# Optimization experiments

Hardware: AMD Instinct MI355X
Metric: run time of the kernel (lower is better)

The kernel has to match this reference:

```python
import jax, jax.numpy as jnp
import numpy as np

EPS = 1e-12  # torch F.normalize default eps


def conv1x1(x, w, b):
    # x: [N,C,H,W], w: [K,C], b: [K]
    return jnp.einsum('nchw,kc->nkhw', x, w) + b[None, :, None, None]


def forward_sa(f1, f2, cw1, cb1, cw2, cb2):
    n, _, h, w = f1.shape
    c1 = conv1x1(f1, cw1, cb1)  # [N,1,H,W]
    c2 = conv1x1(f2, cw2, cb2)
    c1 = jax.nn.softmax(c1.reshape(n, h * w), axis=1).reshape(n, 1, h, w)
    c2 = jax.nn.softmax(c2.reshape(n, h * w), axis=1).reshape(n, 1, h, w)
    return c1 * f1, c2 * f2


def l2norm_ch(x):
    # torch F.normalize(x) -> p=2 over dim=1 with eps clamp
    n = jnp.sqrt(jnp.sum(x * x, axis=1, keepdims=True))
    return x / jnp.maximum(n, EPS)


def forward_ca(f1, f2, pw1, pb1, pw2, pb2):
    N, C, H, W = f1.shape
    f1_cl = conv1x1(f1, pw1, pb1).reshape(N, -1, H * W)  # [N,Cl,HW]
    f2_cl = conv1x1(f2, pw2, pb2).reshape(N, -1, H * W)
    # A[n,p,q] = sum_c f2_cl[n,c,p] * f1_cl[n,c,q]  -> [N,HW,HW]
    A_c = jnp.tanh(jnp.einsum('ncp,ncq->npq', f2_cl, f1_cl))
    f1_v = f1.reshape(N, C, H * W)
    f2_v = f2.reshape(N, C, H * W)
    # f1_hat = f1_v @ A_c^T ; f2_hat = f2_v @ A_c
    f1_hat = jnp.einsum('ncp,nqp->ncq', f1_v, A_c).reshape(N, C, H, W)
    f2_hat = jnp.einsum('ncp,npq->ncq', f2_v, A_c).reshape(N, C, H, W)
    return l2norm_ch(f1_hat), l2norm_ch(f2_hat)


def setup_inputs() -> dict:
    key = jax.random.key(0)
    ks = jax.random.split(key, 10)
    N, C, H, W = 2, 256, 64, 64
    Cl = C // 16
    sc = 1.0 / np.sqrt(C)
    return {
        'f1': jax.random.normal(ks[0], (N, C, H, W), jnp.float32),
        'f2': jax.random.normal(ks[1], (N, C, H, W), jnp.float32),
        'pw1': jax.random.normal(ks[2], (Cl, C), jnp.float32) * sc,
        'pb1': jax.random.normal(ks[3], (Cl,), jnp.float32) * sc,
        'pw2': jax.random.normal(ks[4], (Cl, C), jnp.float32) * sc,
        'pb2': jax.random.normal(ks[5], (Cl,), jnp.float32) * sc,
        'cw1': jax.random.normal(ks[6], (1, C), jnp.float32) * sc,
        'cb1': jax.random.normal(ks[7], (1,), jnp.float32) * sc,
        'cw2': jax.random.normal(ks[8], (1, C), jnp.float32) * sc,
        'cb2': jax.random.normal(ks[9], (1,), jnp.float32) * sc,
    }


def reference(f1, f2, pw1, pb1, pw2, pb2, cw1, cb1, cw2, cb2):
    f1_1, f2_1 = forward_sa(f1, f2, cw1, cb1, cw2, cb2)
    f1_hat, f2_hat = forward_ca(f1_1, f2_1, pw1, pb1, pw2, pb2)
    fp1_hat = jax.nn.relu(f1_hat + f1)
    fp2_hat = jax.nn.relu(f2_hat + f2)
    f1_2, f2_2 = forward_sa(fp1_hat, fp2_hat, cw1, cb1, cw2, cb2)
    # Original calls forward_ca(f1_2, f2_2) again but discards the result
    # and returns (f1_2, f2_2); the dead call is omitted (identical output).
    return (f1_2, f2_2)
```

## Files before the change

kernel.cpp:

```cpp
#include <hip/hip_runtime.h>
#include <hip/hip_bf16.h>
#include <math.h>

#define N_B 2
#define C_CH 256
#define HW_SZ 4096
#define CL_CH 16

typedef __bf16 bf16x8 __attribute__((ext_vector_type(8)));
typedef float f32x4 __attribute__((ext_vector_type(4)));
typedef float f32x16 __attribute__((ext_vector_type(16)));

__device__ __forceinline__ unsigned short f2bf(float x){
  __hip_bfloat16 b = __float2bfloat16(x);
  return *reinterpret_cast<unsigned short*>(&b);
}
__device__ __forceinline__ unsigned int cvtpk(float a, float b){
  unsigned int r;
  asm("v_cvt_pk_bf16_f32 %0, %1, %2" : "=v"(r) : "v"(a), "v"(b));
  return r;
}
__device__ __forceinline__ float tanh_fast(float x){
  float e = __expf(2.0f * x);
  return fmaf(-2.0f, __builtin_amdgcn_rcpf(1.0f + e), 1.0f);
}
__device__ __forceinline__ void gload16(const void* gsrc, void* lds_dst){
  __builtin_amdgcn_global_load_lds(
      (const __attribute__((address_space(1))) unsigned int*)gsrc,
      (__attribute__((address_space(3))) unsigned int*)lds_dst, 16, 0, 0);
}

__global__ void k_conv1(const float* __restrict__ f1, const float* __restrict__ f2,
                        const float* __restrict__ w1, const float* __restrict__ w2,
                        const float* __restrict__ b1, const float* __restrict__ b2,
                        float* __restrict__ cv){
  const int i = blockIdx.z, n = blockIdx.y, t = threadIdx.x;
  const int ql = t & 63, cg = t >> 6;
  const int q = blockIdx.x * 64 + ql;
  const float* f = (i ? f2 : f1) + n * C_CH * HW_SZ;
  const float* w = i ? w2 : w1;
  __shared__ float ws[C_CH];
  __shared__ float red[4][72];
  ws[t] = w[t];
  __syncthreads();
  float acc = 0.f;
  #pragma unroll 8
  for (int c = cg * 64; c < cg * 64 + 64; ++c)
    acc += f[c * HW_SZ + q] * ws[c];
  red[cg][ql] = acc;
  __syncthreads();
  if (t < 64){
    float s = red[0][t] + red[1][t] + red[2][t] + red[3][t] + (i ? b2[0] : b1[0]);
    cv[(i * 2 + n) * HW_SZ + blockIdx.x * 64 + t] = s;
  }
}

__global__ void k_softmax(const float* __restrict__ cv, float* __restrict__ pr){
  const int r = blockIdx.x, t = threadIdx.x;
  const float* x = cv + r * HW_SZ;
  float* y = pr + r * HW_SZ;
  __shared__ float red[256];
  float v[16];
  float m = -1e30f;
  #pragma unroll
  for (int j = 0; j < 16; j++){ v[j] = x[j * 256 + t]; m = fmaxf(m, v[j]); }
  red[t] = m; __syncthreads();
  for (int s = 128; s > 0; s >>= 1){ if (t < s) red[t] = fmaxf(red[t], red[t + s]); __syncthreads(); }
  m = red[0]; __syncthreads();
  float sum = 0.f;
  #pragma unroll
  for (int j = 0; j < 16; j++){ v[j] = __expf(v[j] - m); sum += v[j]; }
  red[t] = sum; __syncthreads();
  for (int s = 128; s > 0; s >>= 1){ if (t < s) red[t] += red[t + s]; __syncthreads(); }
  const float inv = 1.0f / red[0];
  #pragma unroll
  for (int j = 0; j < 16; j++) y[j * 256 + t] = v[j] * inv;
}

__global__ void k_scale_cl(const float* __restrict__ f1, const float* __restrict__ f2,
                           const float* __restrict__ pr,
                           const float* __restrict__ pw1, const float* __restrict__ pw2,
                           const float* __restrict__ pb1, const float* __restrict__ pb2,
                           unsigned short* __restrict__ fs1, unsigned short* __restrict__ fs2,
                           unsigned short* __restrict__ clT1, unsigned short* __restrict__ clT2){
  const int i = blockIdx.z, n = blockIdx.y, t = threadIdx.x;
  const int ql = t & 63, cg = t >> 6;
  const int q = blockIdx.x * 64 + ql;
  const float* f = (i ? f2 : f1) + n * C_CH * HW_SZ;
  unsigned short* fs = (i ? fs2 : fs1) + n * C_CH * HW_SZ;
  unsigned short* clT = (i ? clT2 : clT1) + n * 32 * HW_SZ;
  const float* pw = i ? pw2 : pw1;
  const float* pb = i ? pb2 : pb1;
  __shared__ float wls[CL_CH * C_CH];
  __shared__ float red[4][CL_CH][66];
  #pragma unroll
  for (int j = 0; j < 16; j++) wls[j * 256 + t] = pw[j * 256 + t];
  __syncthreads();
  const float p = pr[(i * 2 + n) * HW_SZ + q];
  float acc[16];
  #pragma unroll
  for (int k = 0; k < 16; k++) acc[k] = 0.f;
  for (int c = cg * 64; c < cg * 64 + 64; ++c){
    float vv = f[c * HW_SZ + q] * p;
    fs[c * HW_SZ + q] = f2bf(vv);
    #pragma unroll
    for (int k = 0; k < 16; k++) acc[k] += wls[k * 256 + c] * vv;
  }
  #pragma unroll
  for (int k = 0; k < 16; k++) red[cg][k][ql] = acc[k];
  __syncthreads();
  #pragma unroll
  for (int j = 0; j < 4; j++){
    int e = j * 256 + t; int k = e >> 6, qq = e & 63;
    float s = red[0][k][qq] + red[1][k][qq] + red[2][k][qq] + red[3][k][qq] + pb[k];
    clT[(blockIdx.x * 64 + qq) * 32 + k] = f2bf(s);
  }
  if (t < 128){
    uint4 zv = {0u, 0u, 0u, 0u};
    int qq = t >> 1, half = t & 1;
    *reinterpret_cast<uint4*>(&clT[(blockIdx.x * 64 + qq) * 32 + 16 + half * 8]) = zv;
  }
}

__global__ __launch_bounds__(512, 4) void k_hat(
    const unsigned short* __restrict__ fs1, const unsigned short* __restrict__ fs2,
    const unsigned short* __restrict__ clT1, const unsigned short* __restrict__ clT2,
    float* __restrict__ hat1, float* __restrict__ hat2,
    float* __restrict__ pt1, float* __restrict__ pt2){
  const int t = threadIdx.x;
  const int bid = blockIdx.x;
  const int xcd = bid & 7, slot = bid >> 3;
  const int z = xcd >> 1;
  const int n = z & 1, i = z >> 1;
  const int x = slot * 2 + (xcd & 1);
  const int qt = x >> 1, ph = x & 1;
  const int q0 = qt * 64;
  const int pbase = ph * 2048;

  const unsigned short* fs = (i ? fs2 : fs1) + n * C_CH * HW_SZ;
  const unsigned short* uT = (i ? clT1 : clT2) + n * 32 * HW_SZ;
  const unsigned short* vT = (i ? clT2 : clT1) + n * 32 * HW_SZ;
  float* out = (ph ? (i ? pt2 : pt1) : (i ? hat2 : hat1)) + n * C_CH * HW_SZ;

  __shared__ __align__(16) unsigned short fsA[2][C_CH * 64];
  __shared__ __align__(16) unsigned short vB[2][64 * 32];
  __shared__ __align__(16) unsigned short aT[64 * 64];

  const int wv = t >> 6, l = t & 63;
  const int g4 = l >> 4, lr16 = l & 15;
  const int g2 = l >> 5, lr32 = l & 31;

  const int pfw = wv & 3;
  const int qf0 = (wv >> 2) * 2;
  const int cblk = wv & 3, qblk = wv >> 2;

  const bf16x8 ub0 = *reinterpret_cast<const bf16x8*>(&uT[(q0 + qf0 * 16 + lr16) * 32 + g4 * 8]);
  const bf16x8 ub1 = *reinterpret_cast<const bf16x8*>(&uT[(q0 + qf0 * 16 + 16 + lr16) * 32 + g4 * 8]);

  f32x16 acc0, acc1;
  #pragma unroll
  for (int r = 0; r < 16; ++r){ acc0[r] = 0.f; acc1[r] = 0.f; }
  const f32x4 zz = {0.f, 0.f, 0.f, 0.f};

  int fs_src[4];
  #pragma unroll
  for (int it = 0; it < 4; ++it){
    int d = it * 512 + t; int c = d >> 3, s = d & 7;
    int u = s ^ (c & 7) ^ (((c >> 3) & 1) << 2);
    fs_src[it] = c * (HW_SZ * 2) + u * 16;
  }
  int vt_src;
  {
    int j = t & 255; int p = j >> 2, s = j & 3;
    int u = s ^ (p & 3) ^ ((p >> 2) & 3);
    vt_src = p * 64 + u * 16;
  }
  int vbr;
  {
    int p = pfw * 16 + lr16;
    vbr = p * 64 + ((g4 ^ (p & 3) ^ ((p >> 2) & 3)) << 4);
  }
  unsigned atw0;
  {
    int qd = qf0 * 16 + lr16;
    int sw = (pfw * 2 + (g4 >> 1)) ^ (qd & 7) ^ (((qd >> 3) & 1) << 2);
    atw0 = qd * 128 + sw * 16 + (g4 & 1) * 8;
  }
  unsigned afo[2], bqo;
  #pragma unroll
  for (int cfi = 0; cfi < 2; ++cfi){
    int crow = cblk * 64 + cfi * 32 + lr32;
    afo[cfi] = crow * 128 + ((g2 ^ (crow & 7) ^ (((crow >> 3) & 1) << 2)) << 4);
  }
  {
    int qrow = qblk * 32 + lr32;
    bqo = qrow * 128 + ((g2 ^ (qrow & 7) ^ (((qrow >> 3) & 1) << 2)) << 4);
  }

  const char* fsb[2] = {(const char*)&fsA[0][0], (const char*)&fsA[1][0]};
  const char* vbb[2] = {(const char*)&vB[0][0], (const char*)&vB[1][0]};
  char* atb = (char*)&aT[0];

  auto stage_fs = [&](unsigned short* dstbase, int p0){
    const char* src = (const char*)fs + p0 * 2;
    #pragma unroll
    for (int it = 0; it < 4; ++it)
      gload16(src + fs_src[it], dstbase + (it * 512 + wv * 64) * 8);
  };
  auto stage_v = [&](unsigned short* dstbase, int p0){
    if (wv < 4)
      gload16((const char*)vT + p0 * 64 + vt_src, dstbase + wv * 512);
  };
  auto dgen = [&](const char* vbB){
    bf16x8 av = *reinterpret_cast<const bf16x8*>(vbB + vbr);
    f32x4 d0 = __builtin_amdgcn_mfma_f32_16x16x32_bf16(av, ub0, zz, 0, 0, 0);
    f32x4 d1 = __builtin_amdgcn_mfma_f32_16x16x32_bf16(av, ub1, zz, 0, 0, 0);
    uint2 pk;
    pk.x = cvtpk(tanh_fast(d0[0]), tanh_fast(d0[1]));
    pk.y = cvtpk(tanh_fast(d0[2]), tanh_fast(d0[3]));
    *reinterpret_cast<uint2*>(atb + atw0) = pk;
    pk.x = cvtpk(tanh_fast(d1[0]), tanh_fast(d1[1]));
    pk.y = cvtpk(tanh_fast(d1[2]), tanh_fast(d1[3]));
    *reinterpret_cast<uint2*>(atb + atw0 + 2048) = pk;
  };
  auto mmain = [&](const char* faB){
    #pragma unroll
    for (int ks = 0; ks < 4; ++ks){
      unsigned kx = (unsigned)(ks << 5);
      bf16x8 b0 = *reinterpret_cast<const bf16x8*>(atb + (bqo ^ kx));
      bf16x8 a0 = *reinterpret_cast<const bf16x8*>(faB + (afo[0] ^ kx));
      bf16x8 a1 = *reinterpret_cast<const bf16x8*>(faB + (afo[1] ^ kx));
      acc0 = __builtin_amdgcn_mfma_f32_32x32x16_bf16(a0, b0, acc0, 0, 0, 0);
      acc1 = __builtin_amdgcn_mfma_f32_32x32x16_bf16(a1, b0, acc1, 0, 0, 0);
    }
  };

  stage_fs(fsA[0], pbase);
  stage_v(vB[0], pbase);
  __syncthreads();

  #pragma unroll 1
  for (int k2 = 0; k2 < 16; ++k2){
    {
      const int p0n = pbase + (2 * k2 + 1) * 64;
      stage_fs(fsA[1], p0n);
      stage_v(vB[1], p0n);
      dgen(vbb[0]);
      asm volatile("s_waitcnt lgkmcnt(0)" ::: "memory");
      __builtin_amdgcn_sched_barrier(0);
      __builtin_amdgcn_s_barrier();
      mmain(fsb[0]);
      __syncthreads();
    }
    {
      const int p0n = pbase + (2 * k2 + 2) * 64;
      stage_fs(fsA[0], p0n);
      stage_v(vB[0], p0n);
      dgen(vbb[1]);
      asm volatile("s_waitcnt lgkmcnt(0)" ::: "memory");
      __builtin_amdgcn_sched_barrier(0);
      __builtin_amdgcn_s_barrier();
      mmain(fsb[1]);
      __syncthreads();
    }
  }

  const int qcol = q0 + qblk * 32 + lr32;
  #pragma unroll
  for (int r = 0; r < 16; ++r){
    int cr = (r & 3) + 8 * (r >> 2) + 4 * g2;
    out[(cblk * 64 + cr) * HW_SZ + qcol] = acc0[r];
    out[(cblk * 64 + 32 + cr) * HW_SZ + qcol] = acc1[r];
  }
}

__global__ void k_norm(float* __restrict__ hat1, float* __restrict__ hat2,
                       const float* __restrict__ pt1, const float* __restrict__ pt2,
                       const float* __restrict__ f1, const float* __restrict__ f2,
                       const float* __restrict__ cw1, const float* __restrict__ cw2,
                       const float* __restrict__ cb1, const float* __restrict__ cb2,
                       float* __restrict__ cv2){
  const int i = blockIdx.z, n = blockIdx.y, t = threadIdx.x;
  const int ql = t & 63, cg = t >> 6;
  const int q = blockIdx.x * 64 + ql;
  float* hat = (i ? hat2 : hat1) + n * C_CH * HW_SZ;
  const float* pt = (i ? pt2 : pt1) + n * C_CH * HW_SZ;
  const float* f = (i ? f2 : f1) + n * C_CH * HW_SZ;
  __shared__ float ws[C_CH];
  __shared__ float red[4][72];
  __shared__ float invs[64];
  ws[t] = (i ? cw2 : cw1)[t];
  __syncthreads();
  float s = 0.f;
  #pragma unroll 8
  for (int c = cg * 64; c < cg * 64 + 64; ++c){
    float h = hat[c * HW_SZ + q] + pt[c * HW_SZ + q];
    s += h * h;
  }
  red[cg][ql] = s; __syncthreads();
  if (t < 64){
    float ss = red[0][t] + red[1][t] + red[2][t] + red[3][t];
    invs[t] = 1.0f / fmaxf(sqrtf(ss), 1e-12f);
  }
  __syncthreads();
  const float inv = invs[ql];
  float ca = 0.f;
  #pragma unroll 8
  for (int c = cg * 64; c < cg * 64 + 64; ++c){
    float h = hat[c * HW_SZ + q] + pt[c * HW_SZ + q];
    float vv = fmaxf(h * inv + f[c * HW_SZ + q], 0.0f);
    hat[c * HW_SZ + q] = vv;
    ca += ws[c] * vv;
  }
  red[cg][ql] = ca; __syncthreads();
  if (t < 64){
    float ss = red[0][t] + red[1][t] + red[2][t] + red[3][t] + (i ? cb2[0] : cb1[0]);
    cv2[(i * 2 + n) * HW_SZ + blockIdx.x * 64 + t] = ss;
  }
}

__global__ void k_final(const float* __restrict__ fp1, const float* __restrict__ fp2,
                        const float* __restrict__ pr2, float* __restrict__ outp){
  const int i = blockIdx.z;
  const int idx4 = (blockIdx.x * 256 + threadIdx.x) * 4;
  const int n = idx4 >> 20;
  const int q = idx4 & (HW_SZ - 1);
  const float* fp = i ? fp2 : fp1;
  float4 vv = *reinterpret_cast<const float4*>(&fp[idx4]);
  float4 pp = *reinterpret_cast<const float4*>(&pr2[(i * 2 + n) * HW_SZ + q]);
  float4 o; o.x = vv.x * pp.x; o.y = vv.y * pp.y; o.z = vv.z * pp.z; o.w = vv.w * pp.w;
  *reinterpret_cast<float4*>(&outp[i * (C_CH * HW_SZ * N_B) + idx4]) = o;
}

extern "C" void kernel_launch(void* const* d_in, const int* in_sizes, int n_in,
                              void* d_out, int out_size, void* d_ws, size_t ws_size,
                              hipStream_t stream){
  const float* f1  = (const float*)d_in[0];
  const float* f2  = (const float*)d_in[1];
  const float* pw1 = (const float*)d_in[2];
  const float* pb1 = (const float*)d_in[3];
  const float* pw2 = (const float*)d_in[4];
  const float* pb2 = (const float*)d_in[5];
  const float* cw1 = (const float*)d_in[6];
  const float* cb1 = (const float*)d_in[7];
  const float* cw2 = (const float*)d_in[8];
  const float* cb2 = (const float*)d_in[9];
  float* ws = (float*)d_ws;
  float* HAT1 = ws;
  float* HAT2 = ws + 2097152;
  float* PT1  = ws + 4194304;
  float* PT2  = ws + 6291456;
  unsigned short* FS1 = (unsigned short*)(ws + 8388608);
  unsigned short* FS2 = (unsigned short*)(ws + 9437184);
  unsigned short* CLT1 = (unsigned short*)(ws + 10485760);
  unsigned short* CLT2 = (unsigned short*)(ws + 10616832);
  float* CV1  = ws + 10747904;
  float* PR1  = ws + 10764288;
  float* CV2  = ws + 10780672;
  float* PR2  = ws + 10797056;
  float* outp = (float*)d_out;

  k_conv1   <<<dim3(64, 2, 2), 256, 0, stream>>>(f1, f2, cw1, cw2, cb1, cb2, CV1);
  k_softmax <<<4, 256, 0, stream>>>(CV1, PR1);
  k_scale_cl<<<dim3(64, 2, 2), 256, 0, stream>>>(f1, f2, PR1, pw1, pw2, pb1, pb2,
                                                 FS1, FS2, CLT1, CLT2);
  k_hat     <<<512, 512, 0, stream>>>(FS1, FS2, CLT1, CLT2, HAT1, HAT2, PT1, PT2);
  k_norm    <<<dim3(64, 2, 2), 256, 0, stream>>>(HAT1, HAT2, PT1, PT2, f1, f2,
                                                 cw1, cw2, cb1, cb2, CV2);
  k_softmax <<<4, 256, 0, stream>>>(CV2, PR2);
  k_final   <<<dim3(2048, 1, 2), 256, 0, stream>>>(HAT1, HAT2, PR2, outp);
}
```

Baseline: 103.9 us.

## Retile k_hat to 128x256 output tiles with 4-way split over p

The k_hat GEMM now has each block compute a 128-channel by 256-position output tile, with each wave owning a 64x64 sub-tile through four 32x32 MFMA accumulators. The reduction over p is split four ways instead of two. The larger tile gives more MFMA work per LDS load and regenerates the tanh attention tile fewer times per output column. The cost is two extra partial-sum buffers: one placed in the output buffer as scratch and one in the workspace. k_norm must therefore read four partials instead of two, which adds global memory traffic.

Result: slower. 153.0 us (+47.4%).

```diff
diff --git a/kernel.cpp b/kernel.cpp
--- a/kernel.cpp
+++ b/kernel.cpp
@@ -126,75 +126,88 @@
     const unsigned short* __restrict__ fs1, const unsigned short* __restrict__ fs2,
     const unsigned short* __restrict__ clT1, const unsigned short* __restrict__ clT2,
     float* __restrict__ hat1, float* __restrict__ hat2,
-    float* __restrict__ pt1, float* __restrict__ pt2){
+    float* __restrict__ pt1, float* __restrict__ pt2,
+    float* __restrict__ q2, float* __restrict__ q3){
   const int t = threadIdx.x;
   const int bid = blockIdx.x;
   const int xcd = bid & 7, slot = bid >> 3;
   const int z = xcd >> 1;
   const int n = z & 1, i = z >> 1;
   const int x = slot * 2 + (xcd & 1);
-  const int qt = x >> 1, ph = x & 1;
-  const int q0 = qt * 64;
-  const int pbase = ph * 2048;
+  const int ph = x & 3;
+  const int cs = (x >> 2) & 1;
+  const int qt = x >> 3;
+  const int q0 = qt * 256;
+  const int c0 = cs * 128;
+  const int pbase = ph * 1024;
 
   const unsigned short* fs = (i ? fs2 : fs1) + n * C_CH * HW_SZ;
   const unsigned short* uT = (i ? clT1 : clT2) + n * 32 * HW_SZ;
   const unsigned short* vT = (i ? clT2 : clT1) + n * 32 * HW_SZ;
-  float* out = (ph ? (i ? pt2 : pt1) : (i ? hat2 : hat1)) + n * C_CH * HW_SZ;
-
-  __shared__ __align__(16) unsigned short fsA[2][C_CH * 64];
+  float* out;
+  {
+    float* o0 = (i ? hat2 : hat1) + n * C_CH * HW_SZ;
+    float* o1 = (i ? pt2 : pt1) + n * C_CH * HW_SZ;
+    float* o2 = q2 + (i * 2 + n) * C_CH * HW_SZ;
+    float* o3 = q3 + (i * 2 + n) * C_CH * HW_SZ;
+    out = (ph == 0) ? o0 : (ph == 1) ? o1 : (ph == 2) ? o2 : o3;
+  }
+
+  __shared__ __align__(16) unsigned short fsA[2][128 * 64];
   __shared__ __align__(16) unsigned short vB[2][64 * 32];
-  __shared__ __align__(16) unsigned short aT[64 * 64];
+  __shared__ __align__(16) unsigned short aT[256 * 64];
 
   const int wv = t >> 6, l = t & 63;
   const int g4 = l >> 4, lr16 = l & 15;
   const int g2 = l >> 5, lr32 = l & 31;
 
-  const int pfw = wv & 3;
-  const int qf0 = (wv >> 2) * 2;
-  const int cblk = wv & 3, qblk = wv >> 2;
-
-  const bf16x8 ub0 = *reinterpret_cast<const bf16x8*>(&uT[(q0 + qf0 * 16 + lr16) * 32 + g4 * 8]);
-  const bf16x8 ub1 = *reinterpret_cast<const bf16x8*>(&uT[(q0 + qf0 * 16 + 16 + lr16) * 32 + g4 * 8]);
-
-  f32x16 acc0, acc1;
-  #pragma unroll
-  for (int r = 0; r < 16; ++r){ acc0[r] = 0.f; acc1[r] = 0.f; }
+  const int cblk = wv & 1, qblk = wv >> 1;
+
+  const bf16x8 ub0 = *reinterpret_cast<const bf16x8*>(&uT[(q0 + wv * 32 + lr16) * 32 + g4 * 8]);
+  const bf16x8 ub1 = *reinterpret_cast<const bf16x8*>(&uT[(q0 + wv * 32 + 16 + lr16) * 32 + g4 * 8]);
+
+  f32x16 acc00, acc01, acc10, acc11;
+  #pragma unroll
+  for (int r = 0; r < 16; ++r){ acc00[r] = 0.f; acc01[r] = 0.f; acc10[r] = 0.f; acc11[r] = 0.f; }
   const f32x4 zz = {0.f, 0.f, 0.f, 0.f};
 
-  int fs_src[4];
-  #pragma unroll
-  for (int it = 0; it < 4; ++it){
-    int d = it * 512 + t; int c = d >> 3, s = d & 7;
-    int u = s ^ (c & 7) ^ (((c >> 3) & 1) << 2);
-    fs_src[it] = c * (HW_SZ * 2) + u * 16;
+  int fs_src[2];
+  #pragma unroll
+  for (int it = 0; it < 2; ++it){
+    int d = it * 512 + t; int c = d >> 3, sl = d & 7;
+    int u = sl ^ (c & 7) ^ (((c >> 3) & 1) << 2) ^ (((c >> 4) & 1) << 1);
+    fs_src[it] = (c0 + c) * (HW_SZ * 2) + u * 16;
   }
   int vt_src;
   {
-    int j = t & 255; int p = j >> 2, s = j & 3;
-    int u = s ^ (p & 3) ^ ((p >> 2) & 3);
+    int j = t & 255; int p = j >> 2, sl = j & 3;
+    int u = sl ^ (p & 3) ^ ((p >> 2) & 3);
     vt_src = p * 64 + u * 16;
   }
-  int vbr;
+  int vbr0;
   {
-    int p = pfw * 16 + lr16;
-    vbr = p * 64 + ((g4 ^ (p & 3) ^ ((p >> 2) & 3)) << 4);
-  }
-  unsigned atw0;
+    int p = lr16;
+    vbr0 = p * 64 + ((g4 ^ (p & 3) ^ ((p >> 2) & 3)) << 4);
+  }
+  unsigned atw00, atw01;
   {
-    int qd = qf0 * 16 + lr16;
-    int sw = (pfw * 2 + (g4 >> 1)) ^ (qd & 7) ^ (((qd >> 3) & 1) << 2);
-    atw0 = qd * 128 + sw * 16 + (g4 & 1) * 8;
-  }
-  unsigned afo[2], bqo;
-  #pragma unroll
-  for (int cfi = 0; cfi < 2; ++cfi){
-    int crow = cblk * 64 + cfi * 32 + lr32;
-    afo[cfi] = crow * 128 + ((g2 ^ (crow & 7) ^ (((crow >> 3) & 1) << 2)) << 4);
-  }
-  {
-    int qrow = qblk * 32 + lr32;
-    bqo = qrow * 128 + ((g2 ^ (qrow & 7) ^ (((qrow >> 3) & 1) << 2)) << 4);
+    int qd = wv * 32 + lr16;
+    int sw = (g4 >> 1) ^ (qd & 7) ^ (((qd >> 3) & 1) << 2) ^ (((qd >> 4) & 1) << 1);
+    atw00 = qd * 128 + sw * 16 + (g4 & 1) * 8;
+    atw01 = (atw00 + 2048) ^ 32;
+  }
+  unsigned afo[2], bqo[2];
+  #pragma unroll
+  for (int cf = 0; cf < 2; ++cf){
+    int crow = cblk * 64 + cf * 32 + lr32;
+    afo[cf] = crow * 128 +
+      ((g2 ^ (crow & 7) ^ (((crow >> 3) & 1) << 2) ^ (((crow >> 4) & 1) << 1)) << 4);
+  }
+  #pragma unroll
+  for (int qf = 0; qf < 2; ++qf){
+    int qrow = qblk * 64 + qf * 32 + lr32;
+    bqo[qf] = qrow * 128 +
+      ((g2 ^ (qrow & 7) ^ (((qrow >> 3) & 1) << 2) ^ (((qrow >> 4) & 1) << 1)) << 4);
   }
 
   const char* fsb[2] = {(const char*)&fsA[0][0], (const char*)&fsA[1][0]};
@@ -204,7 +217,7 @@
   auto stage_fs = [&](unsigned short* dstbase, int p0){
     const char* src = (const char*)fs + p0 * 2;
     #pragma unroll
-    for (int it = 0; it < 4; ++it)
+    for (int it = 0; it < 2; ++it)
       gload16(src + fs_src[it], dstbase + (it * 512 + wv * 64) * 8);
   };
   auto stage_v = [&](unsigned short* dstbase, int p0){
@@ -212,26 +225,32 @@
       gload16((const char*)vT + p0 * 64 + vt_src, dstbase + wv * 512);
   };
   auto dgen = [&](const char* vbB){
-    bf16x8 av = *reinterpret_cast<const bf16x8*>(vbB + vbr);
-    f32x4 d0 = __builtin_amdgcn_mfma_f32_16x16x32_bf16(av, ub0, zz, 0, 0, 0);
-    f32x4 d1 = __builtin_amdgcn_mfma_f32_16x16x32_bf16(av, ub1, zz, 0, 0, 0);
-    uint2 pk;
-    pk.x = cvtpk(tanh_fast(d0[0]), tanh_fast(d0[1]));
-    pk.y = cvtpk(tanh_fast(d0[2]), tanh_fast(d0[3]));
-    *reinterpret_cast<uint2*>(atb + atw0) = pk;
-    pk.x = cvtpk(tanh_fast(d1[0]), tanh_fast(d1[1]));
-    pk.y = cvtpk(tanh_fast(d1[2]), tanh_fast(d1[3]));
-    *reinterpret_cast<uint2*>(atb + atw0 + 2048) = pk;
+    #pragma unroll
+    for (int pf = 0; pf < 4; ++pf){
+      bf16x8 av = *reinterpret_cast<const bf16x8*>(vbB + vbr0 + pf * 1024);
+      f32x4 d0 = __builtin_amdgcn_mfma_f32_16x16x32_bf16(av, ub0, zz, 0, 0, 0);
+      f32x4 d1 = __builtin_amdgcn_mfma_f32_16x16x32_bf16(av, ub1, zz, 0, 0, 0);
+      uint2 pk0, pk1;
+      pk0.x = cvtpk(tanh_fast(d0[0]), tanh_fast(d0[1]));
+      pk0.y = cvtpk(tanh_fast(d0[2]), tanh_fast(d0[3]));
+      pk1.x = cvtpk(tanh_fast(d1[0]), tanh_fast(d1[1]));
+      pk1.y = cvtpk(tanh_fast(d1[2]), tanh_fast(d1[3]));
+      *reinterpret_cast<uint2*>(atb + (atw00 ^ (unsigned)(pf << 5))) = pk0;
+      *reinterpret_cast<uint2*>(atb + (atw01 ^ (unsigned)(pf << 5))) = pk1;
+    }
   };
   auto mmain = [&](const char* faB){
     #pragma unroll
     for (int ks = 0; ks < 4; ++ks){
       unsigned kx = (unsigned)(ks << 5);
-      bf16x8 b0 = *reinterpret_cast<const bf16x8*>(atb + (bqo ^ kx));
       bf16x8 a0 = *reinterpret_cast<const bf16x8*>(faB + (afo[0] ^ kx));
       bf16x8 a1 = *reinterpret_cast<const bf16x8*>(faB + (afo[1] ^ kx));
-      acc0 = __builtin_amdgcn_mfma_f32_32x32x16_bf16(a0, b0, acc0, 0, 0, 0);
-      acc1 = __builtin_amdgcn_mfma_f32_32x32x16_bf16(a1, b0, acc1, 0, 0, 0);
+      bf16x8 b0 = *reinterpret_cast<const bf16x8*>(atb + (bqo[0] ^ kx));
+      bf16x8 b1 = *reinterpret_cast<const bf16x8*>(atb + (bqo[1] ^ kx));
+      acc00 = __builtin_amdgcn_mfma_f32_32x32x16_bf16(a0, b0, acc00, 0, 0, 0);
+      acc01 = __builtin_amdgcn_mfma_f32_32x32x16_bf16(a0, b1, acc01, 0, 0, 0);
+      acc10 = __builtin_amdgcn_mfma_f32_32x32x16_bf16(a1, b0, acc10, 0, 0, 0);
+      acc11 = __builtin_amdgcn_mfma_f32_32x32x16_bf16(a1, b1, acc11, 0, 0, 0);
     }
   };
 
@@ -240,11 +259,10 @@
   __syncthreads();
 
   #pragma unroll 1
-  for (int k2 = 0; k2 < 16; ++k2){
+  for (int k2 = 0; k2 < 8; ++k2){
     {
-      const int p0n = pbase + (2 * k2 + 1) * 64;
-      stage_fs(fsA[1], p0n);
-      stage_v(vB[1], p0n);
+      stage_fs(fsA[1], pbase + (2 * k2 + 1) * 64);
+      stage_v(vB[1], pbase + (2 * k2 + 1) * 64);
       dgen(vbb[0]);
       asm volatile("s_waitcnt lgkmcnt(0)" ::: "memory");
       __builtin_amdgcn_sched_barrier(0);
@@ -253,9 +271,8 @@
       __syncthreads();
     }
     {
-      const int p0n = pbase + (2 * k2 + 2) * 64;
-      stage_fs(fsA[0], p0n);
-      stage_v(vB[0], p0n);
+      stage_fs(fsA[0], pbase + (2 * k2 + 2) * 64);
+      stage_v(vB[0], pbase + (2 * k2 + 2) * 64);
       dgen(vbb[1]);
       asm volatile("s_waitcnt lgkmcnt(0)" ::: "memory");
       __builtin_amdgcn_sched_barrier(0);
@@ -265,17 +282,21 @@
     }
   }
 
-  const int qcol = q0 + qblk * 32 + lr32;
+  const int qcol = q0 + qblk * 64 + lr32;
+  const int cbase = c0 + cblk * 64;
   #pragma unroll
   for (int r = 0; r < 16; ++r){
     int cr = (r & 3) + 8 * (r >> 2) + 4 * g2;
-    out[(cblk * 64 + cr) * HW_SZ + qcol] = acc0[r];
-    out[(cblk * 64 + 32 + cr) * HW_SZ + qcol] = acc1[r];
+    out[(cbase + cr) * HW_SZ + qcol] = acc00[r];
+    out[(cbase + cr) * HW_SZ + qcol + 32] = acc01[r];
+    out[(cbase + 32 + cr) * HW_SZ + qcol] = acc10[r];
+    out[(cbase + 32 + cr) * HW_SZ + qcol + 32] = acc11[r];
   }
 }
 
 __global__ void k_norm(float* __restrict__ hat1, float* __restrict__ hat2,
                        const float* __restrict__ pt1, const float* __restrict__ pt2,
+                       const float* __restrict__ q2, const float* __restrict__ q3,
                        const float* __restrict__ f1, const float* __restrict__ f2,
                        const float* __restrict__ cw1, const float* __restrict__ cw2,
                        const float* __restrict__ cb1, const float* __restrict__ cb2,
@@ -285,6 +306,8 @@
   const int q = blockIdx.x * 64 + ql;
   float* hat = (i ? hat2 : hat1) + n * C_CH * HW_SZ;
   const float* pt = (i ? pt2 : pt1) + n * C_CH * HW_SZ;
+  const float* p2 = q2 + (i * 2 + n) * C_CH * HW_SZ;
+  const float* p3 = q3 + (i * 2 + n) * C_CH * HW_SZ;
   const float* f = (i ? f2 : f1) + n * C_CH * HW_SZ;
   __shared__ float ws[C_CH];
   __shared__ float red[4][72];
@@ -294,7 +317,8 @@
   float s = 0.f;
   #pragma unroll 8
   for (int c = cg * 64; c < cg * 64 + 64; ++c){
-    float h = hat[c * HW_SZ + q] + pt[c * HW_SZ + q];
+    int idx = c * HW_SZ + q;
+    float h = (hat[idx] + pt[idx]) + (p2[idx] + p3[idx]);
     s += h * h;
   }
   red[cg][ql] = s; __syncthreads();
@@ -307,9 +331,10 @@
   float ca = 0.f;
   #pragma unroll 8
   for (int c = cg * 64; c < cg * 64 + 64; ++c){
-    float h = hat[c * HW_SZ + q] + pt[c * HW_SZ + q];
-    float vv = fmaxf(h * inv + f[c * HW_SZ + q], 0.0f);
-    hat[c * HW_SZ + q] = vv;
+    int idx = c * HW_SZ + q;
+    float h = (hat[idx] + pt[idx]) + (p2[idx] + p3[idx]);
+    float vv = fmaxf(h * inv + f[idx], 0.0f);
+    hat[idx] = vv;
     ca += ws[c] * vv;
   }
   red[cg][ql] = ca; __syncthreads();
@@ -346,26 +371,28 @@
   const float* cw2 = (const float*)d_in[8];
   const float* cb2 = (const float*)d_in[9];
   float* ws = (float*)d_ws;
+  float* outp = (float*)d_out;
   float* HAT1 = ws;
   float* HAT2 = ws + 2097152;
   float* PT1  = ws + 4194304;
   float* PT2  = ws + 6291456;
-  unsigned short* FS1 = (unsigned short*)(ws + 8388608);
-  unsigned short* FS2 = (unsigned short*)(ws + 9437184);
-  unsigned short* CLT1 = (unsigned short*)(ws + 10485760);
-  unsigned short* CLT2 = (unsigned short*)(ws + 10616832);
-  float* CV1  = ws + 10747904;
-  float* PR1  = ws + 10764288;
-  float* CV2  = ws + 10780672;
-  float* PR2  = ws + 10797056;
-  float* outp = (float*)d_out;
+  float* Q3   = ws + 8388608;
+  unsigned short* FS1 = (unsigned short*)(ws + 12582912);
+  unsigned short* FS2 = (unsigned short*)(ws + 13631488);
+  unsigned short* CLT1 = (unsigned short*)(ws + 14680064);
+  unsigned short* CLT2 = (unsigned short*)(ws + 14811136);
+  float* CV1  = ws + 14942208;
+  float* PR1  = ws + 14958592;
+  float* CV2  = ws + 14974976;
+  float* PR2  = ws + 14991360;
+  float* Q2   = outp;
 
   k_conv1   <<<dim3(64, 2, 2), 256, 0, stream>>>(f1, f2, cw1, cw2, cb1, cb2, CV1);
   k_softmax <<<4, 256, 0, stream>>>(CV1, PR1);
   k_scale_cl<<<dim3(64, 2, 2), 256, 0, stream>>>(f1, f2, PR1, pw1, pw2, pb1, pb2,
                                                  FS1, FS2, CLT1, CLT2);
-  k_hat     <<<512, 512, 0, stream>>>(FS1, FS2, CLT1, CLT2, HAT1, HAT2, PT1, PT2);
-  k_norm    <<<dim3(64, 2, 2), 256, 0, stream>>>(HAT1, HAT2, PT1, PT2, f1, f2,
+  k_hat     <<<512, 512, 0, stream>>>(FS1, FS2, CLT1, CLT2, HAT1, HAT2, PT1, PT2, Q2, Q3);
+  k_norm    <<<dim3(64, 2, 2), 256, 0, stream>>>(HAT1, HAT2, PT1, PT2, Q2, Q3, f1, f2,
                                                  cw1, cw2, cb1, cb2, CV2);
   k_softmax <<<4, 256, 0, stream>>>(CV2, PR2);
   k_final   <<<dim3(2048, 1, 2), 256, 0, stream>>>(HAT1, HAT2, PR2, outp);
```

## Load V fragments directly into registers, double-buffer A tile, cache hat in norm

Applied to the files above, without the earlier changes.

In k_hat, V operand fragments are now loaded from global memory straight into registers one step ahead, replacing the LDS staging buffer. The tanh attention tile becomes double-buffered, so generating the next tile overlaps the main MFMA loop and the explicit lgkmcnt wait plus barrier go away. In k_norm, each thread keeps its 32 summed hat+pt values in registers so the second pass does not re-read hat and pt. That kernel also launches twice as many blocks with 32 columns each. Costs: higher register pressure and more LDS for the second A tile, and the V loads are less coalesced than the staged ones.

After: 107.7 us. 3.7% more time.

```diff
diff --git a/kernel.cpp b/kernel.cpp
--- a/kernel.cpp
+++ b/kernel.cpp
@@ -143,8 +143,7 @@
   float* out = (ph ? (i ? pt2 : pt1) : (i ? hat2 : hat1)) + n * C_CH * HW_SZ;
 
   __shared__ __align__(16) unsigned short fsA[2][C_CH * 64];
-  __shared__ __align__(16) unsigned short vB[2][64 * 32];
-  __shared__ __align__(16) unsigned short aT[64 * 64];
+  __shared__ __align__(16) unsigned short aT[2][64 * 64];
 
   const int wv = t >> 6, l = t & 63;
   const int g4 = l >> 4, lr16 = l & 15;
@@ -165,21 +164,12 @@
   int fs_src[4];
   #pragma unroll
   for (int it = 0; it < 4; ++it){
-    int d = it * 512 + t; int c = d >> 3, s = d & 7;
-    int u = s ^ (c & 7) ^ (((c >> 3) & 1) << 2);
+    int d = it * 512 + t; int c = d >> 3, sl = d & 7;
+    int u = sl ^ (c & 7) ^ (((c >> 3) & 1) << 2);
     fs_src[it] = c * (HW_SZ * 2) + u * 16;
   }
-  int vt_src;
-  {
-    int j = t & 255; int p = j >> 2, s = j & 3;
-    int u = s ^ (p & 3) ^ ((p >> 2) & 3);
-    vt_src = p * 64 + u * 16;
-  }
-  int vbr;
-  {
-    int p = pfw * 16 + lr16;
-    vbr = p * 64 + ((g4 ^ (p & 3) ^ ((p >> 2) & 3)) << 4);
-  }
+  const char* vbase = (const char*)vT;
+  const int vgo = (pfw * 16 + lr16) * 64 + g4 * 16;
   unsigned atw0;
   {
     int qd = qf0 * 16 + lr16;
@@ -188,46 +178,41 @@
   }
   unsigned afo[2], bqo;
   #pragma unroll
-  for (int cfi = 0; cfi < 2; ++cfi){
-    int crow = cblk * 64 + cfi * 32 + lr32;
-    afo[cfi] = crow * 128 + ((g2 ^ (crow & 7) ^ (((crow >> 3) & 1) << 2)) << 4);
+  for (int cf = 0; cf < 2; ++cf){
+    int crow = cblk * 64 + cf * 32 + lr32;
+    afo[cf] = crow * 128 + ((g2 ^ (crow & 7) ^ (((crow >> 3) & 1) << 2)) << 4);
   }
   {
     int qrow = qblk * 32 + lr32;
     bqo = qrow * 128 + ((g2 ^ (qrow & 7) ^ (((qrow >> 3) & 1) << 2)) << 4);
   }
 
-  const char* fsb[2] = {(const char*)&fsA[0][0], (const char*)&fsA[1][0]};
-  const char* vbb[2] = {(const char*)&vB[0][0], (const char*)&vB[1][0]};
-  char* atb = (char*)&aT[0];
-
+  auto vload = [&](int kk) -> uint4 {
+    return *reinterpret_cast<const uint4*>(vbase + (pbase + kk * 64) * 64 + vgo);
+  };
   auto stage_fs = [&](unsigned short* dstbase, int p0){
     const char* src = (const char*)fs + p0 * 2;
     #pragma unroll
     for (int it = 0; it < 4; ++it)
       gload16(src + fs_src[it], dstbase + (it * 512 + wv * 64) * 8);
   };
-  auto stage_v = [&](unsigned short* dstbase, int p0){
-    if (wv < 4)
-      gload16((const char*)vT + p0 * 64 + vt_src, dstbase + wv * 512);
-  };
-  auto dgen = [&](const char* vbB){
-    bf16x8 av = *reinterpret_cast<const bf16x8*>(vbB + vbr);
+  auto dgen = [&](uint4 vr, char* atB){
+    bf16x8 av = *reinterpret_cast<bf16x8*>(&vr);
     f32x4 d0 = __builtin_amdgcn_mfma_f32_16x16x32_bf16(av, ub0, zz, 0, 0, 0);
     f32x4 d1 = __builtin_amdgcn_mfma_f32_16x16x32_bf16(av, ub1, zz, 0, 0, 0);
-    uint2 pk;
-    pk.x = cvtpk(tanh_fast(d0[0]), tanh_fast(d0[1]));
-    pk.y = cvtpk(tanh_fast(d0[2]), tanh_fast(d0[3]));
-    *reinterpret_cast<uint2*>(atb + atw0) = pk;
-    pk.x = cvtpk(tanh_fast(d1[0]), tanh_fast(d1[1]));
-    pk.y = cvtpk(tanh_fast(d1[2]), tanh_fast(d1[3]));
-    *reinterpret_cast<uint2*>(atb + atw0 + 2048) = pk;
+    uint2 pk0, pk1;
+    pk0.x = cvtpk(tanh_fast(d0[0]), tanh_fast(d0[1]));
+    pk0.y = cvtpk(tanh_fast(d0[2]), tanh_fast(d0[3]));
+    pk1.x = cvtpk(tanh_fast(d1[0]), tanh_fast(d1[1]));
+    pk1.y = cvtpk(tanh_fast(d1[2]), tanh_fast(d1[3]));
+    *reinterpret_cast<uint2*>(atB + atw0) = pk0;
+    *reinterpret_cast<uint2*>(atB + atw0 + 2048) = pk1;
   };
-  auto mmain = [&](const char* faB){
+  auto mmain = [&](const char* faB, const char* atB){
     #pragma unroll
     for (int ks = 0; ks < 4; ++ks){
       unsigned kx = (unsigned)(ks << 5);
-      bf16x8 b0 = *reinterpret_cast<const bf16x8*>(atb + (bqo ^ kx));
+      bf16x8 b0 = *reinterpret_cast<const bf16x8*>(atB + (bqo ^ kx));
       bf16x8 a0 = *reinterpret_cast<const bf16x8*>(faB + (afo[0] ^ kx));
       bf16x8 a1 = *reinterpret_cast<const bf16x8*>(faB + (afo[1] ^ kx));
       acc0 = __builtin_amdgcn_mfma_f32_32x32x16_bf16(a0, b0, acc0, 0, 0, 0);
@@ -235,32 +220,28 @@
     }
   };
 
+  uint4 va = vload(0);
+  uint4 vb = vload(1);
   stage_fs(fsA[0], pbase);
-  stage_v(vB[0], pbase);
+  dgen(va, (char*)aT[0]);
   __syncthreads();
 
   #pragma unroll 1
   for (int k2 = 0; k2 < 16; ++k2){
     {
-      const int p0n = pbase + (2 * k2 + 1) * 64;
-      stage_fs(fsA[1], p0n);
-      stage_v(vB[1], p0n);
-      dgen(vbb[0]);
-      asm volatile("s_waitcnt lgkmcnt(0)" ::: "memory");
-      __builtin_amdgcn_sched_barrier(0);
-      __builtin_amdgcn_s_barrier();
-      mmain(fsb[0]);
+      const int k = 2 * k2;
+      stage_fs(fsA[1], pbase + (k + 1) * 64);
+      va = vload(k + 2);
+      dgen(vb, (char*)aT[1]);
+      mmain((const char*)fsA[0], (const char*)aT[0]);
       __syncthreads();
     }
     {
-      const int p0n = pbase + (2 * k2 + 2) * 64;
-      stage_fs(fsA[0], p0n);
-      stage_v(vB[0], p0n);
-      dgen(vbb[1]);
-      asm volatile("s_waitcnt lgkmcnt(0)" ::: "memory");
-      __builtin_amdgcn_sched_barrier(0);
-      __builtin_amdgcn_s_barrier();
-      mmain(fsb[1]);
+      const int k = 2 * k2 + 1;
+      stage_fs(fsA[0], pbase + (k + 1) * 64);
+      vb = vload(k + 2);
+      dgen(va, (char*)aT[0]);
+      mmain((const char*)fsA[1], (const char*)aT[1]);
       __syncthreads();
     }
   }
@@ -281,41 +262,48 @@
                        const float* __restrict__ cb1, const float* __restrict__ cb2,
                        float* __restrict__ cv2){
   const int i = blockIdx.z, n = blockIdx.y, t = threadIdx.x;
-  const int ql = t & 63, cg = t >> 6;
-  const int q = blockIdx.x * 64 + ql;
+  const int ql = t & 31, cg = t >> 5;
+  const int q = blockIdx.x * 32 + ql;
   float* hat = (i ? hat2 : hat1) + n * C_CH * HW_SZ;
   const float* pt = (i ? pt2 : pt1) + n * C_CH * HW_SZ;
   const float* f = (i ? f2 : f1) + n * C_CH * HW_SZ;
   __shared__ float ws[C_CH];
-  __shared__ float red[4][72];
-  __shared__ float invs[64];
+  __shared__ float red[8][36];
+  __shared__ float invs[32];
   ws[t] = (i ? cw2 : cw1)[t];
   __syncthreads();
+  float hc[32];
   float s = 0.f;
-  #pragma unroll 8
-  for (int c = cg * 64; c < cg * 64 + 64; ++c){
+  #pragma unroll
+  for (int j = 0; j < 32; ++j){
+    int c = cg * 32 + j;
     float h = hat[c * HW_SZ + q] + pt[c * HW_SZ + q];
+    hc[j] = h;
     s += h * h;
   }
   red[cg][ql] = s; __syncthreads();
-  if (t < 64){
-    float ss = red[0][t] + red[1][t] + red[2][t] + red[3][t];
+  if (t < 32){
+    float ss = 0.f;
+    #pragma unroll
+    for (int g = 0; g < 8; ++g) ss += red[g][t];
     invs[t] = 1.0f / fmaxf(sqrtf(ss), 1e-12f);
   }
   __syncthreads();
   const float inv = invs[ql];
   float ca = 0.f;
-  #pragma unroll 8
-  for (int c = cg * 64; c < cg * 64 + 64; ++c){
-    float h = hat[c * HW_SZ + q] + pt[c * HW_SZ + q];
-    float vv = fmaxf(h * inv + f[c * HW_SZ + q], 0.0f);
+  #pragma unroll
+  for (int j = 0; j < 32; ++j){
+    int c = cg * 32 + j;
+    float vv = fmaxf(hc[j] * inv + f[c * HW_SZ + q], 0.0f);
     hat[c * HW_SZ + q] = vv;
     ca += ws[c] * vv;
   }
   red[cg][ql] = ca; __syncthreads();
-  if (t < 64){
-    float ss = red[0][t] + red[1][t] + red[2][t] + red[3][t] + (i ? cb2[0] : cb1[0]);
-    cv2[(i * 2 + n) * HW_SZ + blockIdx.x * 64 + t] = ss;
+  if (t < 32){
+    float ss = (i ? cb2[0] : cb1[0]);
+    #pragma unroll
+    for (int g = 0; g < 8; ++g) ss += red[g][t];
+    cv2[(i * 2 + n) * HW_SZ + blockIdx.x * 32 + t] = ss;
   }
 }
 
@@ -365,8 +353,8 @@
   k_scale_cl<<<dim3(64, 2, 2), 256, 0, stream>>>(f1, f2, PR1, pw1, pw2, pb1, pb2,
                                                  FS1, FS2, CLT1, CLT2);
   k_hat     <<<512, 512, 0, stream>>>(FS1, FS2, CLT1, CLT2, HAT1, HAT2, PT1, PT2);
-  k_norm    <<<dim3(64, 2, 2), 256, 0, stream>>>(HAT1, HAT2, PT1, PT2, f1, f2,
-                                                 cw1, cw2, cb1, cb2, CV2);
+  k_norm    <<<dim3(128, 2, 2), 256, 0, stream>>>(HAT1, HAT2, PT1, PT2, f1, f2,
+                                                  cw1, cw2, cb1, cb2, CV2);
   k_softmax <<<4, 256, 0, stream>>>(CV2, PR2);
   k_final   <<<dim3(2048, 1, 2), 256, 0, stream>>>(HAT1, HAT2, PR2, outp);
 }
```
